# Performance work log

Hardware: AMD Instinct MI355X
Metric: run time of the kernel (lower is better)

The kernel has to match this reference:

```python
import jax, jax.numpy as jnp
import numpy as np

B, T, DM, H, D = 2, 2048, 1024, 16, 64
SCALE = D ** -0.5


def setup_inputs() -> dict:
    key = jax.random.key(0)
    ks = jax.random.split(key, 7)
    std = DM ** -0.5
    inp = {
        "x": jax.random.normal(ks[0], (B, T, DM), dtype=jnp.float32),
        "Wq_re": jax.random.normal(ks[1], (DM, H * D), dtype=jnp.float32) * std,
        "Wq_im": jax.random.normal(ks[2], (DM, H * D), dtype=jnp.float32) * std,
        "Wk_re": jax.random.normal(ks[3], (DM, H * D), dtype=jnp.float32) * std,
        "Wk_im": jax.random.normal(ks[4], (DM, H * D), dtype=jnp.float32) * std,
        "Wv": jax.random.normal(ks[5], (DM, H * D), dtype=jnp.float32) * std,
        "Wo": jax.random.normal(ks[6], (H * D, DM), dtype=jnp.float32) * std,
    }
    # standard RoPE angle cache: theta[t, d] = t * 10000^(-d/D)
    inv_freq = 1.0 / (10000.0 ** (np.arange(D, dtype=np.float32) / D))
    ang = np.arange(T, dtype=np.float32)[:, None] * inv_freq[None, :]
    inp["cos"] = jnp.asarray(np.cos(ang))
    inp["sin"] = jnp.asarray(np.sin(ang))
    return inp


def _split(x, W):
    # [B,T,DM] @ [DM,H*D] -> [B,H,T,D]
    return (x @ W).reshape(B, T, H, D).transpose(0, 2, 1, 3)


def reference(x, Wq_re, Wq_im, Wk_re, Wk_im, Wv, Wo, cos, sin):
    q_re, q_im = _split(x, Wq_re), _split(x, Wq_im)
    k_re, k_im = _split(x, Wk_re), _split(x, Wk_im)

    # complex RoPE: rotate (re, im) by e^{i*theta}; cos/sin broadcast over b,h
    c = cos[None, None]  # [1,1,T,D]
    s = sin[None, None]
    q_re, q_im = q_re * c - q_im * s, q_re * s + q_im * c
    k_re, k_im = k_re * c - k_im * s, k_re * s + k_im * c

    # Hermitian inner product real part: q_re.k_re + q_im.k_im
    scores = (jnp.einsum("bhqd,bhkd->bhqk", q_re, k_re)
              + jnp.einsum("bhqd,bhkd->bhqk", q_im, k_im)) * SCALE

    causal = jnp.tril(jnp.ones((T, T), dtype=bool))
    scores = jnp.where(causal[None, None], scores, -jnp.inf)
    weights = jax.nn.softmax(scores, axis=-1)

    v = _split(x, Wv)
    out = jnp.einsum("bhqk,bhkd->bhqd", weights, v)  # [B,H,T,D]
    out = out.transpose(0, 2, 1, 3).reshape(B, T, H * D)
    return out @ Wo
```

## Files before the change

### kernel.cpp

```cpp
#include <hip/hip_runtime.h>
#include <math.h>

#define SCALE_ 0.125f

typedef _Float16 half_t;
typedef __attribute__((ext_vector_type(8))) _Float16 f16x8;
typedef __attribute__((ext_vector_type(4))) _Float16 f16x4;
typedef __attribute__((ext_vector_type(4))) float f32x4;

#define AS1 __attribute__((address_space(1)))
#define AS3 __attribute__((address_space(3)))

__device__ __forceinline__ f32x4 mfma16(f16x8 a, f16x8 b, f32x4 c) {
  return __builtin_amdgcn_mfma_f32_16x16x32_f16(a, b, c, 0, 0, 0);
}
__device__ __forceinline__ void gload16(const void* g, void* l) {
  __builtin_amdgcn_global_load_lds((const AS1 void*)g, (AS3 void*)l, 16, 0, 0);
}
__device__ __forceinline__ void split2(float f, half_t* h, half_t* l) {
  half_t hh = (half_t)f;
  *h = hh;
  *l = (half_t)(f - (float)hh);
}

__global__ __launch_bounds__(256) void convw_kernel(
    const float* __restrict__ W0, const float* __restrict__ W1,
    const float* __restrict__ W2, const float* __restrict__ W3,
    const float* __restrict__ W4, const float* __restrict__ W5,
    half_t* __restrict__ wh, half_t* __restrict__ wl)
{
  const int z = blockIdx.z;
  const float* W = (z == 0) ? W0 : (z == 1) ? W1 : (z == 2) ? W2
                  : (z == 3) ? W3 : (z == 4) ? W4 : W5;
  half_t* outh = wh + z * 1048576;
  half_t* outl = wl + z * 1048576;
  const int n0 = blockIdx.x * 32, k0 = blockIdx.y * 32;
  const int t = threadIdx.x, r = t >> 3, c4 = (t & 7) * 4;
  __shared__ float lds[32][33];
  float4 v = *(const float4*)&W[(k0 + r) * 1024 + n0 + c4];
  lds[r][c4 + 0] = v.x; lds[r][c4 + 1] = v.y;
  lds[r][c4 + 2] = v.z; lds[r][c4 + 3] = v.w;
  __syncthreads();
  f16x4 oh, ol;
#pragma unroll
  for (int j = 0; j < 4; ++j) {
    const float f = lds[c4 + j][r];
    half_t hv, lv; split2(f, &hv, &lv);
    oh[j] = hv; ol[j] = lv;
  }
  *(f16x4*)&outh[(n0 + r) * 1024 + k0 + c4] = oh;
  *(f16x4*)&outl[(n0 + r) * 1024 + k0 + c4] = ol;
}

__global__ __launch_bounds__(256) void convx_kernel(
    const float* __restrict__ x, half_t* __restrict__ xh, half_t* __restrict__ xl)
{
  const int i = (blockIdx.x * 256 + threadIdx.x) * 4;
  float4 v = *(const float4*)&x[i];
  float vv[4] = {v.x, v.y, v.z, v.w};
  f16x4 oh, ol;
#pragma unroll
  for (int j = 0; j < 4; ++j) {
    half_t hv, lv; split2(vv[j], &hv, &lv);
    oh[j] = hv; ol[j] = lv;
  }
  *(f16x4*)&xh[i] = oh;
  *(f16x4*)&xl[i] = ol;
}

__global__ __launch_bounds__(256) void gemm_kernel(
    const half_t* __restrict__ Agh, const half_t* __restrict__ Agl,
    const half_t* __restrict__ wh, const half_t* __restrict__ wl,
    half_t* __restrict__ qth, half_t* __restrict__ qtl,
    half_t* __restrict__ kth, half_t* __restrict__ ktl,
    half_t* __restrict__ vTh, half_t* __restrict__ vTl,
    float* __restrict__ outp, int final_mode)
{
  __shared__ half_t Ash[4096], Asl[4096], Bsh[4096], Bsl[4096];
  const int z = blockIdx.z;
  const int widx = final_mode ? 5 : z;
  const half_t* Bth = wh + widx * 1048576;
  const half_t* Btl = wl + widx * 1048576;

  const int n0 = blockIdx.x * 128, m0 = blockIdx.y * 128;
  const int tid = threadIdx.x, lane = tid & 63, wid = tid >> 6;
  const int wr = wid >> 1, wc = wid & 1, l15 = lane & 15, l4 = lane >> 4;

  f32x4 acc[4][4];
#pragma unroll
  for (int i = 0; i < 4; ++i)
#pragma unroll
    for (int j = 0; j < 4; ++j) acc[i][j] = (f32x4){0.f, 0.f, 0.f, 0.f};

  const int s0 = wid * 64 + lane, s1 = s0 + 256;
  const int r0 = s0 >> 2, c0 = (s0 & 3) * 8;
  const int r1 = s1 >> 2, c1 = (s1 & 3) * 8;
  half_t* Ah0 = Ash + wid * 512;        half_t* Ah1 = Ash + 2048 + wid * 512;
  half_t* Al0 = Asl + wid * 512;        half_t* Al1 = Asl + 2048 + wid * 512;
  half_t* Bh0 = Bsh + wid * 512;        half_t* Bh1 = Bsh + 2048 + wid * 512;
  half_t* Bl0 = Bsl + wid * 512;        half_t* Bl1 = Bsl + 2048 + wid * 512;

  for (int k0 = 0; k0 < 1024; k0 += 32) {
    __syncthreads();
    gload16(Agh + (m0 + r0) * 1024 + k0 + c0, Ah0);
    gload16(Agh + (m0 + r1) * 1024 + k0 + c1, Ah1);
    gload16(Agl + (m0 + r0) * 1024 + k0 + c0, Al0);
    gload16(Agl + (m0 + r1) * 1024 + k0 + c1, Al1);
    gload16(Bth + (n0 + r0) * 1024 + k0 + c0, Bh0);
    gload16(Bth + (n0 + r1) * 1024 + k0 + c1, Bh1);
    gload16(Btl + (n0 + r0) * 1024 + k0 + c0, Bl0);
    gload16(Btl + (n0 + r1) * 1024 + k0 + c1, Bl1);
    __syncthreads();
    f16x8 ah[4], al[4], bh[4], bl[4];
#pragma unroll
    for (int i = 0; i < 4; ++i) {
      const int ro = (wr * 64 + i * 16 + l15) * 32 + l4 * 8;
      ah[i] = *(const f16x8*)&Ash[ro];
      al[i] = *(const f16x8*)&Asl[ro];
    }
#pragma unroll
    for (int j = 0; j < 4; ++j) {
      const int ro = (wc * 64 + j * 16 + l15) * 32 + l4 * 8;
      bh[j] = *(const f16x8*)&Bsh[ro];
      bl[j] = *(const f16x8*)&Bsl[ro];
    }
#pragma unroll
    for (int i = 0; i < 4; ++i)
#pragma unroll
      for (int j = 0; j < 4; ++j) {
        acc[i][j] = mfma16(ah[i], bh[j], acc[i][j]);
        acc[i][j] = mfma16(ah[i], bl[j], acc[i][j]);
        acc[i][j] = mfma16(al[i], bh[j], acc[i][j]);
      }
  }

#pragma unroll
  for (int i = 0; i < 4; ++i) {
    const int mb = m0 + wr * 64 + i * 16 + l4 * 4;
#pragma unroll
    for (int j = 0; j < 4; ++j) {
      const int n = n0 + wc * 64 + j * 16 + l15;
      if (final_mode) {
#pragma unroll
        for (int r = 0; r < 4; ++r) outp[(mb + r) * 1024 + n] = acc[i][j][r];
      } else if (z < 4) {
        half_t* dh = (z < 2) ? qth : kth;
        half_t* dl = (z < 2) ? qtl : ktl;
        const int colr = (n >> 6) * 128 + (n & 63) + ((z & 1) ? 64 : 0);
#pragma unroll
        for (int r = 0; r < 4; ++r) {
          half_t hv, lv; split2(acc[i][j][r], &hv, &lv);
          dh[(mb + r) * 2048 + colr] = hv;
          dl[(mb + r) * 2048 + colr] = lv;
        }
      } else {
        const int hh = n >> 6, d = n & 63;
        const int bq = mb >> 11, t = mb & 2047;
        f16x4 vh4, vl4;
#pragma unroll
        for (int r = 0; r < 4; ++r) {
          half_t hv, lv; split2(acc[i][j][r], &hv, &lv);
          vh4[r] = hv; vl4[r] = lv;
        }
        const int off = ((bq * 16 + hh) * 64 + d) * 2048 + t;
        *(f16x4*)&vTh[off] = vh4;
        *(f16x4*)&vTl[off] = vl4;
      }
    }
  }
}

__global__ __launch_bounds__(256) void rope_kernel(
    const half_t* __restrict__ qth, const half_t* __restrict__ qtl,
    const half_t* __restrict__ kth, const half_t* __restrict__ ktl,
    const float* __restrict__ cosb, const float* __restrict__ sinb,
    half_t* __restrict__ qbh, half_t* __restrict__ qbl,
    half_t* __restrict__ kbh, half_t* __restrict__ kbl)
{
  const int z = blockIdx.y;
  const int g = blockIdx.x * 4 + (threadIdx.x >> 6);
  const int d = threadIdx.x & 63;
  const int m = g >> 4, h = g & 15;
  const int b = m >> 11, t = m & 2047;
  const half_t* sh = (z ? kth : qth) + m * 2048 + h * 128;
  const half_t* sl = (z ? ktl : qtl) + m * 2048 + h * 128;
  const float re = (float)sh[d] + (float)sl[d];
  const float im = (float)sh[64 + d] + (float)sl[64 + d];
  const float c = cosb[t * 64 + d], s = sinb[t * 64 + d];
  float rer = re * c - im * s;
  float imr = re * s + im * c;
  if (z == 0) { rer *= SCALE_; imr *= SCALE_; }
  half_t* dh = (z ? kbh : qbh) + ((b * 16 + h) * 2048 + t) * 128;
  half_t* dl = (z ? kbl : qbl) + ((b * 16 + h) * 2048 + t) * 128;
  half_t hv, lv;
  split2(rer, &hv, &lv); dh[d] = hv;      dl[d] = lv;
  split2(imr, &hv, &lv); dh[64 + d] = hv; dl[64 + d] = lv;
}

__global__ __launch_bounds__(256) void attn_kernel(
    const half_t* __restrict__ qbh, const half_t* __restrict__ qbl,
    const half_t* __restrict__ kbh, const half_t* __restrict__ kbl,
    const half_t* __restrict__ vTh, const half_t* __restrict__ vTl,
    half_t* __restrict__ abh, half_t* __restrict__ abl)
{
  const int qt = (int)gridDim.x - 1 - (int)blockIdx.x;
  const int bh = blockIdx.y;
  const int b = bh >> 4, h = bh & 15;
  const int tid = threadIdx.x, lane = tid & 63, w = tid >> 6;
  const int l15 = lane & 15, l4 = lane >> 4;
  const int q0 = qt * 64;

  __shared__ half_t Kh[8192], Kl[8192];
  __shared__ half_t Vh[4096], Vl[4096];
  __shared__ half_t Ph[4096], Pl[4096];

  f16x8 qh[4], ql[4];
  {
    const int qoff = (bh * 2048 + q0 + w * 16 + l15) * 128;
#pragma unroll
    for (int c = 0; c < 4; ++c) {
      qh[c] = *(const f16x8*)(qbh + qoff + c * 32 + l4 * 8);
      ql[c] = *(const f16x8*)(qbl + qoff + c * 32 + l4 * 8);
    }
  }

  f32x4 o[4];
#pragma unroll
  for (int n = 0; n < 4; ++n) o[n] = (f32x4){0.f, 0.f, 0.f, 0.f};
  float mrow[4] = {-3e38f, -3e38f, -3e38f, -3e38f};
  float lrow[4] = {0.f, 0.f, 0.f, 0.f};

  const half_t* kh_p = kbh + bh * 2048 * 128;
  const half_t* kl_p = kbl + bh * 2048 * 128;
  const half_t* vh_p = vTh + bh * 64 * 2048;
  const half_t* vl_p = vTl + bh * 64 * 2048;

  for (int kt = 0; kt <= qt; ++kt) {
    const int k0 = kt * 64;
    __syncthreads();
    {
      f16x8 kh_[4], kl_[4], vh_[2], vl_[2];
#pragma unroll
      for (int it = 0; it < 4; ++it) {
        const int sIdx = it * 256 + tid, row = sIdx >> 4, slot = sIdx & 15;
        kh_[it] = *(const f16x8*)(kh_p + (k0 + row) * 128 + slot * 8);
        kl_[it] = *(const f16x8*)(kl_p + (k0 + row) * 128 + slot * 8);
      }
#pragma unroll
      for (int it = 0; it < 2; ++it) {
        const int sIdx = it * 256 + tid, row = sIdx >> 3, slot = sIdx & 7;
        vh_[it] = *(const f16x8*)(vh_p + row * 2048 + k0 + slot * 8);
        vl_[it] = *(const f16x8*)(vl_p + row * 2048 + k0 + slot * 8);
      }
#pragma unroll
      for (int it = 0; it < 4; ++it) {
        const int sIdx = it * 256 + tid, row = sIdx >> 4, slot = sIdx & 15;
        const int sp = (slot & 8) | ((slot & 7) ^ (row & 7));
        *(f16x8*)&Kh[row * 128 + sp * 8] = kh_[it];
        *(f16x8*)&Kl[row * 128 + sp * 8] = kl_[it];
      }
#pragma unroll
      for (int it = 0; it < 2; ++it) {
        const int sIdx = it * 256 + tid, row = sIdx >> 3, slot = sIdx & 7;
        const int sp = slot ^ (row & 7);
        *(f16x8*)&Vh[row * 64 + sp * 8] = vh_[it];
        *(f16x8*)&Vl[row * 64 + sp * 8] = vl_[it];
      }
    }
    __syncthreads();

    f32x4 s[4];
#pragma unroll
    for (int n = 0; n < 4; ++n) s[n] = (f32x4){0.f, 0.f, 0.f, 0.f};
#pragma unroll
    for (int c = 0; c < 4; ++c) {
#pragma unroll
      for (int n = 0; n < 4; ++n) {
        const int row = n * 16 + l15;
        const int slot = c * 4 + l4;
        const int sp = (slot & 8) | ((slot & 7) ^ (row & 7));
        const f16x8 kfh = *(const f16x8*)&Kh[row * 128 + sp * 8];
        const f16x8 kfl = *(const f16x8*)&Kl[row * 128 + sp * 8];
        s[n] = mfma16(qh[c], kfh, s[n]);
        s[n] = mfma16(qh[c], kfl, s[n]);
        s[n] = mfma16(ql[c], kfh, s[n]);
      }
    }

    if (kt == qt) {
#pragma unroll
      for (int n = 0; n < 4; ++n)
#pragma unroll
        for (int r = 0; r < 4; ++r)
          if (n * 16 + l15 > w * 16 + l4 * 4 + r) s[n][r] = -3e38f;
    }

#pragma unroll
    for (int r = 0; r < 4; ++r) {
      float mx = fmaxf(fmaxf(s[0][r], s[1][r]), fmaxf(s[2][r], s[3][r]));
      mx = fmaxf(mx, __shfl_xor(mx, 1));
      mx = fmaxf(mx, __shfl_xor(mx, 2));
      mx = fmaxf(mx, __shfl_xor(mx, 4));
      mx = fmaxf(mx, __shfl_xor(mx, 8));
      const float mnew = fmaxf(mrow[r], mx);
      const float alpha = __expf(mrow[r] - mnew);
      float p[4];
#pragma unroll
      for (int n = 0; n < 4; ++n) p[n] = __expf(s[n][r] - mnew);
      float rs = p[0] + p[1] + p[2] + p[3];
      rs += __shfl_xor(rs, 1);
      rs += __shfl_xor(rs, 2);
      rs += __shfl_xor(rs, 4);
      rs += __shfl_xor(rs, 8);
      lrow[r] = lrow[r] * alpha + rs;
      mrow[r] = mnew;
#pragma unroll
      for (int n = 0; n < 4; ++n) o[n][r] *= alpha;
      const int prow = w * 16 + l4 * 4 + r;
#pragma unroll
      for (int n = 0; n < 4; ++n) {
        const int col = n * 16 + l15;
        const int sp = (col >> 3) ^ (prow & 7);
        half_t hv, lv; split2(p[n], &hv, &lv);
        Ph[prow * 64 + sp * 8 + (col & 7)] = hv;
        Pl[prow * 64 + sp * 8 + (col & 7)] = lv;
      }
    }
    __syncthreads();

#pragma unroll
    for (int c = 0; c < 2; ++c) {
      const int prow = w * 16 + l15;
      const int sp = (c * 4 + l4) ^ (prow & 7);
      const f16x8 pfh = *(const f16x8*)&Ph[prow * 64 + sp * 8];
      const f16x8 pfl = *(const f16x8*)&Pl[prow * 64 + sp * 8];
#pragma unroll
      for (int n = 0; n < 4; ++n) {
        const int vrow = n * 16 + l15;
        const int sp2 = (c * 4 + l4) ^ (vrow & 7);
        const f16x8 vfh = *(const f16x8*)&Vh[vrow * 64 + sp2 * 8];
        const f16x8 vfl = *(const f16x8*)&Vl[vrow * 64 + sp2 * 8];
        o[n] = mfma16(pfh, vfh, o[n]);
        o[n] = mfma16(pfh, vfl, o[n]);
        o[n] = mfma16(pfl, vfh, o[n]);
      }
    }
  }

  const int mg = b * 2048 + q0 + w * 16 + l4 * 4;
#pragma unroll
  for (int r = 0; r < 4; ++r) {
    const float inv = 1.0f / lrow[r];
    const int m = mg + r;
#pragma unroll
    for (int n = 0; n < 4; ++n) {
      half_t hv, lv; split2(o[n][r] * inv, &hv, &lv);
      abh[m * 1024 + h * 64 + n * 16 + l15] = hv;
      abl[m * 1024 + h * 64 + n * 16 + l15] = lv;
    }
  }
}

extern "C" void kernel_launch(void* const* d_in, const int* in_sizes, int n_in,
                              void* d_out, int out_size, void* d_ws,
                              size_t ws_size, hipStream_t stream) {
  const float* x    = (const float*)d_in[0];
  const float* Wqre = (const float*)d_in[1];
  const float* Wqim = (const float*)d_in[2];
  const float* Wkre = (const float*)d_in[3];
  const float* Wkim = (const float*)d_in[4];
  const float* Wv   = (const float*)d_in[5];
  const float* Wo   = (const float*)d_in[6];
  const float* cosb = (const float*)d_in[7];
  const float* sinb = (const float*)d_in[8];

  char* w = (char*)d_ws;
  const size_t MB = (size_t)1 << 20;
  half_t* wh6 = (half_t*)(w + 0 * MB);
  half_t* wl6 = (half_t*)(w + 12 * MB);
  half_t* xh  = (half_t*)(w + 24 * MB);
  half_t* xl  = (half_t*)(w + 32 * MB);
  half_t* qth = (half_t*)(w + 40 * MB);
  half_t* qtl = (half_t*)(w + 56 * MB);
  half_t* kth = (half_t*)(w + 72 * MB);
  half_t* ktl = (half_t*)(w + 88 * MB);
  half_t* qbh = (half_t*)(w + 104 * MB);
  half_t* qbl = (half_t*)(w + 120 * MB);
  half_t* kbh = (half_t*)(w + 136 * MB);
  half_t* kbl = (half_t*)(w + 152 * MB);
  half_t* vTh = (half_t*)(w + 168 * MB);
  half_t* vTl = (half_t*)(w + 176 * MB);
  half_t* abh = (half_t*)(w + 40 * MB);
  half_t* abl = (half_t*)(w + 48 * MB);

  dim3 blk(256);
  convw_kernel<<<dim3(32, 32, 6), blk, 0, stream>>>(Wqre, Wqim, Wkre, Wkim, Wv,
                                                    Wo, wh6, wl6);
  convx_kernel<<<dim3(4096), blk, 0, stream>>>(x, xh, xl);
  gemm_kernel<<<dim3(8, 32, 5), blk, 0, stream>>>(xh, xl, wh6, wl6, qth, qtl,
                                                  kth, ktl, vTh, vTl, nullptr, 0);
  rope_kernel<<<dim3(16384, 2), blk, 0, stream>>>(qth, qtl, kth, ktl, cosb,
                                                  sinb, qbh, qbl, kbh, kbl);
  attn_kernel<<<dim3(32, 32), blk, 0, stream>>>(qbh, qbl, kbh, kbl, vTh, vTl,
                                                abh, abl);
  gemm_kernel<<<dim3(8, 32, 1), blk, 0, stream>>>(abh, abl, wh6, wl6, nullptr,
                                                  nullptr, nullptr, nullptr,
                                                  nullptr, nullptr,
                                                  (float*)d_out, 1);
}
```

Measured before the change: 565.9 us.

## Drop split-precision for V and P, read K/V directly from global, reorder blocks

Stores V only as a single fp16 value, without the low-order correction term, and uses a single fp16 P in the PV matmul, cutting that matmul from three MFMAs per step to one. K and V fragments are now loaded straight from global memory into registers instead of being staged through shared memory, which removes the per-tile barriers. Fully masked key sub-tiles on the diagonal are skipped. The grid is flattened to 1D and interleaves long and short query tiles for load balance. The risks are lower precision for V and P, and more global or L2 traffic because K and V are reloaded by each wave.

```diff
diff --git a/kernel.cpp b/kernel.cpp
--- a/kernel.cpp
+++ b/kernel.cpp
@@ -156,15 +156,11 @@
       } else {
         const int hh = n >> 6, d = n & 63;
         const int bq = mb >> 11, t = mb & 2047;
-        f16x4 vh4, vl4;
-#pragma unroll
-        for (int r = 0; r < 4; ++r) {
-          half_t hv, lv; split2(acc[i][j][r], &hv, &lv);
-          vh4[r] = hv; vl4[r] = lv;
-        }
+        f16x4 vh4;
+#pragma unroll
+        for (int r = 0; r < 4; ++r) vh4[r] = (half_t)acc[i][j][r];
         const int off = ((bq * 16 + hh) * 64 + d) * 2048 + t;
         *(f16x4*)&vTh[off] = vh4;
-        *(f16x4*)&vTl[off] = vl4;
       }
     }
   }
@@ -200,23 +196,23 @@
 __global__ __launch_bounds__(256) void attn_kernel(
     const half_t* __restrict__ qbh, const half_t* __restrict__ qbl,
     const half_t* __restrict__ kbh, const half_t* __restrict__ kbl,
-    const half_t* __restrict__ vTh, const half_t* __restrict__ vTl,
+    const half_t* __restrict__ vTh,
     half_t* __restrict__ abh, half_t* __restrict__ abl)
 {
-  const int qt = (int)gridDim.x - 1 - (int)blockIdx.x;
-  const int bh = blockIdx.y;
+  const int i = blockIdx.x;
+  const int bh = i & 31;
+  const int j = i >> 5;
+  const int qt = (i < 512) ? (31 - j) : (j - 16);
   const int b = bh >> 4, h = bh & 15;
   const int tid = threadIdx.x, lane = tid & 63, w = tid >> 6;
   const int l15 = lane & 15, l4 = lane >> 4;
   const int q0 = qt * 64;
 
-  __shared__ half_t Kh[8192], Kl[8192];
-  __shared__ half_t Vh[4096], Vl[4096];
-  __shared__ half_t Ph[4096], Pl[4096];
+  __shared__ half_t Ph[64 * 80];
 
   f16x8 qh[4], ql[4];
   {
-    const int qoff = (bh * 2048 + q0 + w * 16 + l15) * 128;
+    const size_t qoff = ((size_t)bh * 2048 + q0 + w * 16 + l15) * 128;
 #pragma unroll
     for (int c = 0; c < 4; ++c) {
       qh[c] = *(const f16x8*)(qbh + qoff + c * 32 + l4 * 8);
@@ -230,69 +226,41 @@
   float mrow[4] = {-3e38f, -3e38f, -3e38f, -3e38f};
   float lrow[4] = {0.f, 0.f, 0.f, 0.f};
 
-  const half_t* kh_p = kbh + bh * 2048 * 128;
-  const half_t* kl_p = kbl + bh * 2048 * 128;
-  const half_t* vh_p = vTh + bh * 64 * 2048;
-  const half_t* vl_p = vTl + bh * 64 * 2048;
+  const half_t* kh_p = kbh + (size_t)bh * 2048 * 128;
+  const half_t* kl_p = kbl + (size_t)bh * 2048 * 128;
+  const half_t* vh_p = vTh + (size_t)bh * 64 * 2048;
+
+  const int qminw = q0 + w * 16;
+  const int qmaxw = qminw + 15;
 
   for (int kt = 0; kt <= qt; ++kt) {
     const int k0 = kt * 64;
-    __syncthreads();
-    {
-      f16x8 kh_[4], kl_[4], vh_[2], vl_[2];
-#pragma unroll
-      for (int it = 0; it < 4; ++it) {
-        const int sIdx = it * 256 + tid, row = sIdx >> 4, slot = sIdx & 15;
-        kh_[it] = *(const f16x8*)(kh_p + (k0 + row) * 128 + slot * 8);
-        kl_[it] = *(const f16x8*)(kl_p + (k0 + row) * 128 + slot * 8);
-      }
-#pragma unroll
-      for (int it = 0; it < 2; ++it) {
-        const int sIdx = it * 256 + tid, row = sIdx >> 3, slot = sIdx & 7;
-        vh_[it] = *(const f16x8*)(vh_p + row * 2048 + k0 + slot * 8);
-        vl_[it] = *(const f16x8*)(vl_p + row * 2048 + k0 + slot * 8);
-      }
-#pragma unroll
-      for (int it = 0; it < 4; ++it) {
-        const int sIdx = it * 256 + tid, row = sIdx >> 4, slot = sIdx & 15;
-        const int sp = (slot & 8) | ((slot & 7) ^ (row & 7));
-        *(f16x8*)&Kh[row * 128 + sp * 8] = kh_[it];
-        *(f16x8*)&Kl[row * 128 + sp * 8] = kl_[it];
-      }
-#pragma unroll
-      for (int it = 0; it < 2; ++it) {
-        const int sIdx = it * 256 + tid, row = sIdx >> 3, slot = sIdx & 7;
-        const int sp = slot ^ (row & 7);
-        *(f16x8*)&Vh[row * 64 + sp * 8] = vh_[it];
-        *(f16x8*)&Vl[row * 64 + sp * 8] = vl_[it];
-      }
-    }
-    __syncthreads();
+    const bool diag = (kt == qt);
 
     f32x4 s[4];
 #pragma unroll
     for (int n = 0; n < 4; ++n) s[n] = (f32x4){0.f, 0.f, 0.f, 0.f};
 #pragma unroll
-    for (int c = 0; c < 4; ++c) {
-#pragma unroll
-      for (int n = 0; n < 4; ++n) {
-        const int row = n * 16 + l15;
-        const int slot = c * 4 + l4;
-        const int sp = (slot & 8) | ((slot & 7) ^ (row & 7));
-        const f16x8 kfh = *(const f16x8*)&Kh[row * 128 + sp * 8];
-        const f16x8 kfl = *(const f16x8*)&Kl[row * 128 + sp * 8];
+    for (int n = 0; n < 4; ++n) {
+      if (diag && k0 + n * 16 > qmaxw) continue;
+      const half_t* kp  = kh_p + (size_t)(k0 + n * 16 + l15) * 128 + l4 * 8;
+      const half_t* klp = kl_p + (size_t)(k0 + n * 16 + l15) * 128 + l4 * 8;
+#pragma unroll
+      for (int c = 0; c < 4; ++c) {
+        const f16x8 kfh = *(const f16x8*)(kp + c * 32);
+        const f16x8 kfl = *(const f16x8*)(klp + c * 32);
         s[n] = mfma16(qh[c], kfh, s[n]);
         s[n] = mfma16(qh[c], kfl, s[n]);
         s[n] = mfma16(ql[c], kfh, s[n]);
       }
     }
 
-    if (kt == qt) {
+    if (diag) {
 #pragma unroll
       for (int n = 0; n < 4; ++n)
 #pragma unroll
         for (int r = 0; r < 4; ++r)
-          if (n * 16 + l15 > w * 16 + l4 * 4 + r) s[n][r] = -3e38f;
+          if (k0 + n * 16 + l15 > qminw + l4 * 4 + r) s[n][r] = -3e38f;
     }
 
 #pragma unroll
@@ -317,32 +285,26 @@
 #pragma unroll
       for (int n = 0; n < 4; ++n) o[n][r] *= alpha;
       const int prow = w * 16 + l4 * 4 + r;
+      const int pr80 = prow * 80;
+      const int psw = prow & 7;
 #pragma unroll
       for (int n = 0; n < 4; ++n) {
         const int col = n * 16 + l15;
-        const int sp = (col >> 3) ^ (prow & 7);
-        half_t hv, lv; split2(p[n], &hv, &lv);
-        Ph[prow * 64 + sp * 8 + (col & 7)] = hv;
-        Pl[prow * 64 + sp * 8 + (col & 7)] = lv;
-      }
-    }
-    __syncthreads();
-
-#pragma unroll
-    for (int c = 0; c < 2; ++c) {
-      const int prow = w * 16 + l15;
-      const int sp = (c * 4 + l4) ^ (prow & 7);
-      const f16x8 pfh = *(const f16x8*)&Ph[prow * 64 + sp * 8];
-      const f16x8 pfl = *(const f16x8*)&Pl[prow * 64 + sp * 8];
+        const int sp = ((col >> 3) ^ psw) & 7;
+        Ph[pr80 + sp * 8 + (col & 7)] = (half_t)p[n];
+      }
+    }
+
+#pragma unroll
+    for (int kc = 0; kc < 2; ++kc) {
+      const int arow = w * 16 + l15;
+      const int sp = ((kc * 4 + l4) ^ (arow & 7)) & 7;
+      const f16x8 pf = *(const f16x8*)&Ph[arow * 80 + sp * 8];
 #pragma unroll
       for (int n = 0; n < 4; ++n) {
-        const int vrow = n * 16 + l15;
-        const int sp2 = (c * 4 + l4) ^ (vrow & 7);
-        const f16x8 vfh = *(const f16x8*)&Vh[vrow * 64 + sp2 * 8];
-        const f16x8 vfl = *(const f16x8*)&Vl[vrow * 64 + sp2 * 8];
-        o[n] = mfma16(pfh, vfh, o[n]);
-        o[n] = mfma16(pfh, vfl, o[n]);
-        o[n] = mfma16(pfl, vfh, o[n]);
+        const f16x8 vf = *(const f16x8*)(vh_p + (size_t)(n * 16 + l15) * 2048 +
+                                         k0 + kc * 32 + l4 * 8);
+        o[n] = mfma16(pf, vf, o[n]);
       }
     }
   }
@@ -401,8 +363,8 @@
                                                   kth, ktl, vTh, vTl, nullptr, 0);
   rope_kernel<<<dim3(16384, 2), blk, 0, stream>>>(qth, qtl, kth, ktl, cosb,
                                                   sinb, qbh, qbl, kbh, kbl);
-  attn_kernel<<<dim3(32, 32), blk, 0, stream>>>(qbh, qbl, kbh, kbl, vTh, vTl,
-                                                abh, abl);
+  attn_kernel<<<dim3(1024), blk, 0, stream>>>(qbh, qbl, kbh, kbl, vTh, abh,
+                                              abl);
   gemm_kernel<<<dim3(8, 32, 1), blk, 0, stream>>>(abh, abl, wh6, wl6, nullptr,
                                                   nullptr, nullptr, nullptr,
                                                   nullptr, nullptr,
```

New measurement: 623.4 us. +10.2%, slower.
